# Kernel tuning notes

Hardware: AMD Instinct MI355X
Metric: run time of the kernel (lower is better)

Reference implementation:

```python
import jax, jax.numpy as jnp
import numpy as np

N = 100000   # nodes
E = 1600000  # edges
EPS = 1e-5


def _gcn_conv(x, W, b, src, dst, dinv):
    # PyG GCNConv with self-loops: out_i = sum_{j->i} d_j^-1/2 d_i^-1/2 (x_j W) + d_i^-1 (x_i W) + b
    h = x @ W                                   # [N, out]
    coef = dinv[src] * dinv[dst]                # [E]
    agg = jax.ops.segment_sum(h[src] * coef[:, None], dst, num_segments=N)
    agg = agg + h * (dinv * dinv)[:, None]      # self-loop term
    return agg + b


def _bn_eval(x, gamma, beta, mean, var):
    return (x - mean) * jax.lax.rsqrt(var + EPS) * gamma + beta


def setup_inputs() -> dict:
    key = jax.random.key(0)
    ks = jax.random.split(key, 8)
    F_IN, H, C = 128, 256, 32
    inp = {
        "x": jax.random.normal(ks[0], (N, F_IN), dtype=jnp.float32),
        "edge_index": jax.random.randint(ks[1], (2, E), 0, N, dtype=jnp.int64),
        # layer 1
        "W1": jax.random.normal(ks[2], (F_IN, H), dtype=jnp.float32) / np.sqrt(F_IN),
        "b1": jnp.zeros((H,), jnp.float32),
        "g1": jnp.ones((H,), jnp.float32),
        "be1": jnp.zeros((H,), jnp.float32),
        "m1": jax.random.normal(ks[3], (H,), dtype=jnp.float32) * 0.1,
        "v1": jnp.ones((H,), jnp.float32),
        # layer 2
        "W2": jax.random.normal(ks[4], (H, H), dtype=jnp.float32) / np.sqrt(H),
        "b2": jnp.zeros((H,), jnp.float32),
        "g2": jnp.ones((H,), jnp.float32),
        "be2": jnp.zeros((H,), jnp.float32),
        "m2": jax.random.normal(ks[5], (H,), dtype=jnp.float32) * 0.1,
        "v2": jnp.ones((H,), jnp.float32),
        # layer 3
        "W3": jax.random.normal(ks[6], (H, C), dtype=jnp.float32) / np.sqrt(H),
        "b3": jnp.zeros((C,), jnp.float32),
    }
    return inp


def reference(x, edge_index, W1, b1, g1, be1, m1, v1,
              W2, b2, g2, be2, m2, v2, W3, b3):
    src, dst = edge_index[0], edge_index[1]
    # degree with self-loops: in-degree + 1
    deg = jnp.zeros((N,), x.dtype).at[dst].add(1.0) + 1.0
    dinv = jax.lax.rsqrt(deg)

    h = _gcn_conv(x, W1, b1, src, dst, dinv)
    h = jax.nn.relu(_bn_eval(h, g1, be1, m1, v1))
    h = _gcn_conv(h, W2, b2, src, dst, dinv)
    h = jax.nn.relu(_bn_eval(h, g2, be2, m2, v2))
    h = _gcn_conv(h, W3, b3, src, dst, dinv)
    return jax.nn.sigmoid(h)
```

## Files before the change

kernel.cpp:

```cpp
#include <hip/hip_runtime.h>
#include <math.h>

typedef unsigned short u16;
typedef unsigned char u8;
typedef unsigned int u32;
typedef __attribute__((ext_vector_type(8))) __bf16 bfx8;
typedef __attribute__((ext_vector_type(4))) float f32x4;
typedef __attribute__((ext_vector_type(2))) float f32x2;
typedef __attribute__((ext_vector_type(8))) unsigned short us8;
typedef __attribute__((ext_vector_type(4))) unsigned short us4;

__device__ inline float bf2f(u16 u) {
    union { unsigned int i; float f; } v;
    v.i = ((unsigned int)u) << 16;
    return v.f;
}
__device__ inline u16 f2bf(float f) {
    union { float f; unsigned int i; } v;
    v.f = f;
    unsigned int b = v.i;
    return (u16)((b + 0x7FFFu + ((b >> 16) & 1u)) >> 16);
}
__device__ inline u32 bits_of(float f) {
    union { float f; u32 i; } v; v.f = f; return v.i;
}
__device__ inline u32 pkbf(float a, float b) {
    return (bits_of(a) >> 16) | (bits_of(b) & 0xffff0000u);
}
__device__ inline void dec4(u32 d, u32& lo, u32& hi) {
    f32x2 a = __builtin_amdgcn_cvt_pk_f32_fp8(d, false);
    f32x2 b = __builtin_amdgcn_cvt_pk_f32_fp8(d, true);
    lo = pkbf(a[0], a[1]);
    hi = pkbf(b[0], b[1]);
}


__global__ __launch_bounds__(256) void k_hist(const int* __restrict__ ei,
                                              u32* __restrict__ cnt_pb,
                                              int E, int NB, int NBLK) {
    __shared__ u32 h[256];
    int blk = blockIdx.x, tid = threadIdx.x;
    h[tid] = 0;
    __syncthreads();
    int eend = min(E, (blk + 1) * 2048);
    for (int e = blk * 2048 + tid; e < eend; e += 256) {
        int d = ei[E + e];
        atomicAdd(&h[d >> 9], 1u);
    }
    __syncthreads();
    if (tid < NB) cnt_pb[(size_t)tid * NBLK + blk] = h[tid];
}

__global__ __launch_bounds__(1024) void k_scanb(const u32* __restrict__ cnt_pb,
                                                u32* __restrict__ bases_pb,
                                                u32* __restrict__ bkt_tot,
                                                int NBLK) {
    __shared__ u32 lds[1024];
    int b = blockIdx.x, t = threadIdx.x;
    u32 v = (t < NBLK) ? cnt_pb[(size_t)b * NBLK + t] : 0u;
    lds[t] = v;
    __syncthreads();
    for (int off = 1; off < 1024; off <<= 1) {
        u32 x = lds[t];
        u32 y = (t >= off) ? lds[t - off] : 0u;
        __syncthreads();
        lds[t] = x + y;
        __syncthreads();
    }
    if (t < NBLK) bases_pb[(size_t)b * NBLK + t] = lds[t] - v;
    if (t == NBLK - 1) bkt_tot[b] = lds[t];
}

__global__ __launch_bounds__(256) void k_scatter2(const int* __restrict__ ei,
                                                  const u32* __restrict__ bases_pb,
                                                  const u32* __restrict__ bkt_tot,
                                                  u32* __restrict__ bkt_edges,
                                                  int E, int NB, int NBLK) {
    __shared__ u32 cur[256];
    __shared__ u32 bb[256];
    int blk = blockIdx.x, tid = threadIdx.x;
    u32 v = (tid < NB) ? bkt_tot[tid] : 0u;
    bb[tid] = v;
    __syncthreads();
    for (int off = 1; off < 256; off <<= 1) {
        u32 x = bb[tid];
        u32 y = (tid >= off) ? bb[tid - off] : 0u;
        __syncthreads();
        bb[tid] = x + y;
        __syncthreads();
    }
    u32 excl = bb[tid] - v;
    __syncthreads();
    bb[tid] = excl;
    if (tid < NB) cur[tid] = bases_pb[(size_t)tid * NBLK + blk];
    __syncthreads();
    int eend = min(E, (blk + 1) * 2048);
    for (int e = blk * 2048 + tid; e < eend; e += 256) {
        int s = ei[e];
        int d = ei[E + e];
        int b = d >> 9;
        int dl = d & 511;
        u32 off = atomicAdd(&cur[b], 1u);
        bkt_edges[bb[b] + off] = (u32)s | ((u32)dl << 17);
    }
}

__global__ __launch_bounds__(512) void k_bucket(const u32* __restrict__ bkt_edges,
                                                const u32* __restrict__ bkt_tot,
                                                int* __restrict__ row_ptr,
                                                float* __restrict__ dinv,
                                                int* __restrict__ csr_src,
                                                int N, int NB, int E) {
    __shared__ u32 sb[256];
    __shared__ u32 lcnt[512];
    __shared__ u32 lscan[512];
    int b = blockIdx.x, t = threadIdx.x;
    if (t < 256) sb[t] = (t < NB) ? bkt_tot[t] : 0u;
    __syncthreads();
    for (int off = 1; off < 256; off <<= 1) {
        u32 x = 0, y = 0;
        if (t < 256) { x = sb[t]; y = (t >= off) ? sb[t - off] : 0u; }
        __syncthreads();
        if (t < 256) sb[t] = x + y;
        __syncthreads();
    }
    int ce = (int)bkt_tot[b];
    int es = (int)sb[b] - ce;
    int node0 = b << 9;
    lcnt[t] = 0;
    __syncthreads();
    for (int i = t; i < ce; i += 512) {
        u32 p = bkt_edges[es + i];
        atomicAdd(&lcnt[p >> 17], 1u);
    }
    __syncthreads();
    lscan[t] = lcnt[t];
    __syncthreads();
    for (int off = 1; off < 512; off <<= 1) {
        u32 x = lscan[t];
        u32 y = (t >= off) ? lscan[t - off] : 0u;
        __syncthreads();
        lscan[t] = x + y;
        __syncthreads();
    }
    u32 excl = lscan[t] - lcnt[t];
    int node = node0 + t;
    if (node < N) {
        row_ptr[node] = es + (int)excl;
        dinv[node] = rsqrtf((float)lcnt[t] + 1.0f);
    }
    if (b == 0 && t == 0) row_ptr[N] = E;
    __syncthreads();
    lscan[t] = excl;
    __syncthreads();
    for (int i = t; i < ce; i += 512) {
        u32 p = bkt_edges[es + i];
        int dl = (int)(p >> 17);
        int src = (int)(p & 0x1FFFFu);
        u32 pos = atomicAdd(&lscan[dl], 1u);
        csr_src[es + pos] = src;
    }
}

__global__ __launch_bounds__(256) void k_prep(
    const float* __restrict__ x, u8* __restrict__ xq, const float* __restrict__ dinv, int n4,
    const float* __restrict__ W1, u16* __restrict__ Wt1,
    const float* __restrict__ W2, u16* __restrict__ Wt2,
    const float* __restrict__ W3, u16* __restrict__ Wt3,
    const float* __restrict__ b1, const float* __restrict__ g1, const float* __restrict__ be1,
    const float* __restrict__ m1, const float* __restrict__ v1,
    float* __restrict__ s1, float* __restrict__ t1,
    const float* __restrict__ b2, const float* __restrict__ g2, const float* __restrict__ be2,
    const float* __restrict__ m2, const float* __restrict__ v2,
    float* __restrict__ s2, float* __restrict__ t2)
{
    int i = blockIdx.x * blockDim.x + threadIdx.x;
    if (i < n4) {
        float d = dinv[i >> 5];
        float4 v = *(const float4*)(x + (size_t)i * 4);
        u32 pk = 0;
        pk = __builtin_amdgcn_cvt_pk_fp8_f32(v.x * d, v.y * d, pk, false);
        pk = __builtin_amdgcn_cvt_pk_fp8_f32(v.z * d, v.w * d, pk, true);
        *(u32*)(xq + (size_t)i * 4) = pk;
        return;
    }
    int j = i - n4;
    if (j < 128 * 256) {
        int k = j / 256, f = j % 256;
        Wt1[(size_t)f * 128 + k] = f2bf(W1[j]);
    } else if (j < 128 * 256 + 256 * 256) {
        int j2 = j - 128 * 256;
        int k = j2 / 256, f = j2 % 256;
        Wt2[(size_t)f * 256 + k] = f2bf(W2[j2]);
    } else if (j < 128 * 256 + 256 * 256 + 256 * 32) {
        int j3 = j - (128 * 256 + 256 * 256);
        int k = j3 / 32, f = j3 % 32;
        Wt3[(size_t)f * 256 + k] = f2bf(W3[j3]);
    } else {
        int k = j - (128 * 256 + 256 * 256 + 256 * 32);
        if (k < 256) {
            float sc = g1[k] * rsqrtf(v1[k] + 1e-5f);
            s1[k] = sc;
            t1[k] = (b1[k] - m1[k]) * sc + be1[k];
        } else if (k < 512) {
            int kk = k - 256;
            float sc = g2[kk] * rsqrtf(v2[kk] + 1e-5f);
            s2[kk] = sc;
            t2[kk] = (b2[kk] - m2[kk]) * sc + be2[kk];
        }
    }
}

template<int K, int FT, int MODE, bool AFP8, int MINW>
__global__ __launch_bounds__(256, MINW) void g_mfma_lds(
    const void* __restrict__ Av, const u16* __restrict__ Wt,
    void* __restrict__ Cv, int M, int Ftot,
    const float* __restrict__ s, const float* __restrict__ t,
    const float* __restrict__ dinv, int nTiles)
{
    constexpr bool DOBN = (MODE == 1) || (MODE == 3);
    constexpr bool CF8  = (MODE >= 3);
    constexpr int BK  = 128;
    constexpr int SA  = BK + 8;
    constexpr int NH  = K / BK;
    constexpr int NKH = BK / 32;
    constexpr int NF  = FT / 16;
    constexpr int EB  = CF8 ? 1 : 2;
    constexpr int SCB = FT * EB + 16;
    constexpr int EBa = AFP8 ? 1 : 2;
    constexpr int CR  = (BK * EBa) / 16;
    constexpr int LIT = (64 * CR) / 256;

    __shared__ u16 Asmem[2][64 * SA];
    __shared__ u8  Cs8[64 * SCB];

    const u8* Ab = (const u8*)Av;
    int tid = threadIdx.x;
    int w = tid >> 6, l = tid & 63;
    int lr = l & 15, koff8 = (l >> 4) * 8;
    int col0 = blockIdx.y * FT;

    bfx8 bfr[NH][NKH][NF];
    {
        const u16* wp = Wt + (size_t)(col0 + lr) * K + koff8;
        #pragma unroll
        for (int h = 0; h < NH; ++h)
            #pragma unroll
            for (int kk = 0; kk < NKH; ++kk)
                #pragma unroll
                for (int c = 0; c < NF; ++c)
                    bfr[h][kk][c] = *(const bfx8*)(wp + (size_t)c * 16 * K + h * BK + kk * 32);
    }

    int myT = (blockIdx.x < nTiles) ? ((nTiles - 1 - (int)blockIdx.x) / (int)gridDim.x + 1) : 0;
    int NM = myT * NH;
    if (NM == 0) return;

    f32x4 acc[NF];
    #pragma unroll
    for (int c = 0; c < NF; ++c) acc[c] = (f32x4){0.f, 0.f, 0.f, 0.f};

    uint4 rga[LIT];

    auto loadA = [&](int r0, int hh) {
        #pragma unroll
        for (int j = 0; j < LIT; ++j) {
            int cid = j * 256 + tid;
            int row = cid / CR, ch = cid % CR;
            int gr = r0 + row; if (gr > M - 1) gr = M - 1;
            rga[j] = *(const uint4*)(Ab + (size_t)gr * K * EBa + (size_t)hh * BK * EBa + ch * 16);
        }
    };
    auto writeA = [&](int buf) {
        #pragma unroll
        for (int j = 0; j < LIT; ++j) {
            int cid = j * 256 + tid;
            int row = cid / CR, ch = cid % CR;
            if (!AFP8) {
                *(uint4*)&Asmem[buf][row * SA + ch * 8] = rga[j];
            } else {
                u32 w0, w1, w2, w3, w4, w5, w6, w7;
                dec4(rga[j].x, w0, w1);
                dec4(rga[j].y, w2, w3);
                dec4(rga[j].z, w4, w5);
                dec4(rga[j].w, w6, w7);
                uint4 lo4; lo4.x = w0; lo4.y = w1; lo4.z = w2; lo4.w = w3;
                uint4 hi4; hi4.x = w4; hi4.y = w5; hi4.z = w6; hi4.w = w7;
                *(uint4*)&Asmem[buf][row * SA + ch * 16] = lo4;
                *(uint4*)&Asmem[buf][row * SA + ch * 16 + 8] = hi4;
            }
        }
    };

    loadA(blockIdx.x * 64, 0);
    writeA(0);
    if (NM > 1) {
        constexpr int gt1 = 1 / NH, h1 = 1 % NH;
        loadA((blockIdx.x + gt1 * gridDim.x) * 64, h1);
    }
    __syncthreads();

    int cur = 0, gm = 0;
    for (int ti = 0; ti < myT; ++ti) {
        int row0g = (blockIdx.x + ti * gridDim.x) * 64;
        #pragma unroll
        for (int h = 0; h < NH; ++h) {
            const u16* ab = &Asmem[cur][0];
            #pragma unroll
            for (int kk = 0; kk < NKH; ++kk) {
                bfx8 af = *(const bfx8*)(ab + (w * 16 + lr) * SA + koff8 + kk * 32);
                #pragma unroll
                for (int c = 0; c < NF; ++c)
                    acc[c] = __builtin_amdgcn_mfma_f32_16x16x32_bf16(af, bfr[h][kk][c], acc[c], 0, 0, 0);
            }
            if (h == NH - 1) {
                int orow = w * 16 + (l >> 4) * 4;
                float dr[4];
                #pragma unroll
                for (int r = 0; r < 4; ++r) {
                    int grow = row0g + orow + r;
                    dr[r] = DOBN ? ((grow < M) ? dinv[grow] : 0.f) : 1.f;
                }
                #pragma unroll
                for (int c = 0; c < NF; ++c) {
                    int gc = col0 + c * 16 + lr;
                    float sc = DOBN ? s[gc] : 0.f;
                    float tc = DOBN ? t[gc] : 0.f;
                    #pragma unroll
                    for (int r = 0; r < 4; ++r) {
                        float v = acc[c][r];
                        if (DOBN) v = fmaxf(v * sc + tc, 0.f) * dr[r];
                        if (CF8) {
                            int enc = __builtin_amdgcn_cvt_pk_fp8_f32(v, v, 0, false);
                            Cs8[(orow + r) * SCB + (c * 16 + lr)] = (u8)(enc & 0xff);
                        } else {
                            *(u16*)&Cs8[(orow + r) * SCB + (c * 16 + lr) * 2] = f2bf(v);
                        }
                    }
                    acc[c] = (f32x4){0.f, 0.f, 0.f, 0.f};
                }
            }
            __syncthreads();
            if (gm + 1 < NM) writeA(cur ^ 1);
            if (h == NH - 1) {
                constexpr int CPR = (FT * EB) / 16;
                constexpr int TOT = 64 * CPR;
                constexpr int CPT = (TOT + 255) / 256;
                u8* C8 = (u8*)Cv;
                #pragma unroll
                for (int j = 0; j < CPT; ++j) {
                    int cid = j * 256 + tid;
                    if (cid < TOT) {
                        int crow = cid / CPR;
                        int cb = (cid % CPR) * 16;
                        int grow = row0g + crow;
                        if (grow < M) {
                            us8 vv = *(const us8*)&Cs8[crow * SCB + cb];
                            *(us8*)(C8 + (size_t)grow * Ftot * EB + (size_t)col0 * EB + cb) = vv;
                        }
                    }
                }
            }
            if (gm + 2 < NM) {
                int g2 = gm + 2;
                int gt2 = g2 / NH, h2 = g2 % NH;
                loadA((blockIdx.x + gt2 * gridDim.x) * 64, h2);
            }
            __syncthreads();
            cur ^= 1; ++gm;
        }
    }
}

__global__ __launch_bounds__(256) void agg_x(const u8* __restrict__ in,
                                             u8* __restrict__ outp,
                                             const int* __restrict__ row_ptr,
                                             const int* __restrict__ csr_src,
                                             const float* __restrict__ dinv,
                                             int nnodes) {
    int tid = threadIdx.x;
    int wv = tid >> 6, lane = tid & 63;
    int half = lane >> 5, l32 = lane & 31;
    int node = (blockIdx.x * 4 + wv) * 2 + half;
    if (node >= nnodes) return;
    int off = l32 * 4;
    const u8* bp = in + off;
    float a0, a1, a2, a3;
    {
        u32 q = *(const u32*)(in + (size_t)node * 128 + off);
        f32x2 p;
        p = __builtin_amdgcn_cvt_pk_f32_fp8(q, false); a0 = p[0]; a1 = p[1];
        p = __builtin_amdgcn_cvt_pk_f32_fp8(q, true);  a2 = p[0]; a3 = p[1];
    }
    int e = row_ptr[node], e1 = row_ptr[node + 1];
    for (; e + 8 <= e1; e += 8) {
        int sx[8];
        #pragma unroll
        for (int q = 0; q < 8; ++q) sx[q] = csr_src[e + q];
        u32 vv[8];
        #pragma unroll
        for (int q = 0; q < 8; ++q) vv[q] = *(const u32*)(bp + (size_t)sx[q] * 128);
        #pragma unroll
        for (int q = 0; q < 8; ++q) {
            f32x2 p;
            p = __builtin_amdgcn_cvt_pk_f32_fp8(vv[q], false); a0 += p[0]; a1 += p[1];
            p = __builtin_amdgcn_cvt_pk_f32_fp8(vv[q], true);  a2 += p[0]; a3 += p[1];
        }
    }
    for (; e < e1; ++e) {
        int s0 = csr_src[e];
        u32 v0 = *(const u32*)(bp + (size_t)s0 * 128);
        f32x2 p;
        p = __builtin_amdgcn_cvt_pk_f32_fp8(v0, false); a0 += p[0]; a1 += p[1];
        p = __builtin_amdgcn_cvt_pk_f32_fp8(v0, true);  a2 += p[0]; a3 += p[1];
    }
    float d = dinv[node];
    u32 pk = 0;
    pk = __builtin_amdgcn_cvt_pk_fp8_f32(a0 * d, a1 * d, pk, false);
    pk = __builtin_amdgcn_cvt_pk_fp8_f32(a2 * d, a3 * d, pk, true);
    *(u32*)(outp + (size_t)node * 128 + off) = pk;
}

__global__ __launch_bounds__(256) void agg_h(const u8* __restrict__ in,
                                             u8* __restrict__ outp,
                                             const int* __restrict__ row_ptr,
                                             const int* __restrict__ csr_src,
                                             const float* __restrict__ dinv,
                                             int nnodes) {
    int tid = threadIdx.x;
    int wv = tid >> 6, lane = tid & 63;
    int half = lane >> 5, l32 = lane & 31;
    int node = (blockIdx.x * 4 + wv) * 2 + half;
    if (node >= nnodes) return;
    int off = l32 * 8;
    const u8* bp = in + off;
    float acc[8];
    {
        uint2 q = *(const uint2*)(in + (size_t)node * 256 + off);
        f32x2 p;
        p = __builtin_amdgcn_cvt_pk_f32_fp8(q.x, false); acc[0] = p[0]; acc[1] = p[1];
        p = __builtin_amdgcn_cvt_pk_f32_fp8(q.x, true);  acc[2] = p[0]; acc[3] = p[1];
        p = __builtin_amdgcn_cvt_pk_f32_fp8(q.y, false); acc[4] = p[0]; acc[5] = p[1];
        p = __builtin_amdgcn_cvt_pk_f32_fp8(q.y, true);  acc[6] = p[0]; acc[7] = p[1];
    }
    int e = row_ptr[node], e1 = row_ptr[node + 1];
    for (; e + 8 <= e1; e += 8) {
        int sx[8];
        #pragma unroll
        for (int q = 0; q < 8; ++q) sx[q] = csr_src[e + q];
        uint2 vv[8];
        #pragma unroll
        for (int q = 0; q < 8; ++q) vv[q] = *(const uint2*)(bp + (size_t)sx[q] * 256);
        #pragma unroll
        for (int q = 0; q < 8; ++q) {
            f32x2 p;
            p = __builtin_amdgcn_cvt_pk_f32_fp8(vv[q].x, false); acc[0] += p[0]; acc[1] += p[1];
            p = __builtin_amdgcn_cvt_pk_f32_fp8(vv[q].x, true);  acc[2] += p[0]; acc[3] += p[1];
            p = __builtin_amdgcn_cvt_pk_f32_fp8(vv[q].y, false); acc[4] += p[0]; acc[5] += p[1];
            p = __builtin_amdgcn_cvt_pk_f32_fp8(vv[q].y, true);  acc[6] += p[0]; acc[7] += p[1];
        }
    }
    for (; e < e1; ++e) {
        int s0 = csr_src[e];
        uint2 v0 = *(const uint2*)(bp + (size_t)s0 * 256);
        f32x2 p;
        p = __builtin_amdgcn_cvt_pk_f32_fp8(v0.x, false); acc[0] += p[0]; acc[1] += p[1];
        p = __builtin_amdgcn_cvt_pk_f32_fp8(v0.x, true);  acc[2] += p[0]; acc[3] += p[1];
        p = __builtin_amdgcn_cvt_pk_f32_fp8(v0.y, false); acc[4] += p[0]; acc[5] += p[1];
        p = __builtin_amdgcn_cvt_pk_f32_fp8(v0.y, true);  acc[6] += p[0]; acc[7] += p[1];
    }
    float d = dinv[node];
    u32 w0 = 0, w1 = 0;
    w0 = __builtin_amdgcn_cvt_pk_fp8_f32(acc[0] * d, acc[1] * d, w0, false);
    w0 = __builtin_amdgcn_cvt_pk_fp8_f32(acc[2] * d, acc[3] * d, w0, true);
    w1 = __builtin_amdgcn_cvt_pk_fp8_f32(acc[4] * d, acc[5] * d, w1, false);
    w1 = __builtin_amdgcn_cvt_pk_fp8_f32(acc[6] * d, acc[7] * d, w1, true);
    uint2 o; o.x = w0; o.y = w1;
    *(uint2*)(outp + (size_t)node * 256 + off) = o;
}

__global__ __launch_bounds__(256) void agg32_sig(const u8* __restrict__ zq,
                                                 float* __restrict__ out,
                                                 const int* __restrict__ row_ptr,
                                                 const int* __restrict__ csr_src,
                                                 const float* __restrict__ dinv,
                                                 const float* __restrict__ b3,
                                                 int nnodes) {
    int tid = threadIdx.x;
    int grp = tid >> 3, l8 = tid & 7;
    int node = blockIdx.x * 32 + grp;
    if (node >= nnodes) return;
    int off = l8 * 4;
    const u8* bp = zq + off;
    float a0, a1, a2, a3;
    {
        u32 q = *(const u32*)(zq + (size_t)node * 32 + off);
        f32x2 p;
        p = __builtin_amdgcn_cvt_pk_f32_fp8(q, false); a0 = p[0]; a1 = p[1];
        p = __builtin_amdgcn_cvt_pk_f32_fp8(q, true);  a2 = p[0]; a3 = p[1];
    }
    int e = row_ptr[node], e1 = row_ptr[node + 1];
    for (; e + 8 <= e1; e += 8) {
        int sx[8];
        #pragma unroll
        for (int q = 0; q < 8; ++q) sx[q] = csr_src[e + q];
        u32 vv[8];
        #pragma unroll
        for (int q = 0; q < 8; ++q) vv[q] = *(const u32*)(bp + (size_t)sx[q] * 32);
        #pragma unroll
        for (int q = 0; q < 8; ++q) {
            f32x2 p;
            p = __builtin_amdgcn_cvt_pk_f32_fp8(vv[q], false); a0 += p[0]; a1 += p[1];
            p = __builtin_amdgcn_cvt_pk_f32_fp8(vv[q], true);  a2 += p[0]; a3 += p[1];
        }
    }
    for (; e < e1; ++e) {
        int s0 = csr_src[e];
        u32 v0 = *(const u32*)(bp + (size_t)s0 * 32);
        f32x2 p;
        p = __builtin_amdgcn_cvt_pk_f32_fp8(v0, false); a0 += p[0]; a1 += p[1];
        p = __builtin_amdgcn_cvt_pk_f32_fp8(v0, true);  a2 += p[0]; a3 += p[1];
    }
    float d = dinv[node];
    int fb = l8 * 4;
    float4 o;
    o.x = 1.f / (1.f + expf(-(a0 * d + b3[fb + 0])));
    o.y = 1.f / (1.f + expf(-(a1 * d + b3[fb + 1])));
    o.z = 1.f / (1.f + expf(-(a2 * d + b3[fb + 2])));
    o.w = 1.f / (1.f + expf(-(a3 * d + b3[fb + 3])));
    *(float4*)(out + (size_t)node * 32 + fb) = o;
}


extern "C" void kernel_launch(void* const* d_in, const int* in_sizes, int n_in,
                              void* d_out, int out_size, void* d_ws, size_t ws_size,
                              hipStream_t stream) {
    const float* x  = (const float*)d_in[0];
    const int*   ei = (const int*)d_in[1];
    const float* W1 = (const float*)d_in[2];
    const float* b1 = (const float*)d_in[3];
    const float* g1 = (const float*)d_in[4];
    const float* be1 = (const float*)d_in[5];
    const float* m1 = (const float*)d_in[6];
    const float* v1 = (const float*)d_in[7];
    const float* W2 = (const float*)d_in[8];
    const float* b2 = (const float*)d_in[9];
    const float* g2 = (const float*)d_in[10];
    const float* be2 = (const float*)d_in[11];
    const float* m2 = (const float*)d_in[12];
    const float* v2 = (const float*)d_in[13];
    const float* W3 = (const float*)d_in[14];
    const float* b3 = (const float*)d_in[15];
    float* out = (float*)d_out;

    const int N = in_sizes[0] / 128;
    const int E = in_sizes[1] / 2;

    const int NB = (N + 511) >> 9;
    const int NBLK = (E + 2047) / 2048;

    char* w = (char*)d_ws;
    auto alloc = [&](size_t bytes) -> void* {
        void* p = (void*)w;
        w += (bytes + 255) & ~(size_t)255;
        return p;
    };
    int* row_ptr   = (int*)alloc((size_t)(N + 1) * 4);
    float* dinv    = (float*)alloc((size_t)N * 4);
    u32* cnt_pb    = (u32*)alloc((size_t)NB * NBLK * 4);
    u32* bases_pb  = (u32*)alloc((size_t)NB * NBLK * 4);
    u32* bkt_tot   = (u32*)alloc((size_t)NB * 4);
    u32* bkt_edges = (u32*)alloc((size_t)E * 4);
    float* s1 = (float*)alloc(256 * 4);
    float* t1 = (float*)alloc(256 * 4);
    float* s2 = (float*)alloc(256 * 4);
    float* t2 = (float*)alloc(256 * 4);
    u16* Wt1 = (u16*)alloc((size_t)128 * 256 * 2);
    u16* Wt2 = (u16*)alloc((size_t)256 * 256 * 2);
    u16* Wt3 = (u16*)alloc((size_t)256 * 32 * 2);
    int* csr_src = (int*)alloc((size_t)E * 4);
    u8*  xq   = (u8*)alloc((size_t)N * 128);
    u8*  xa   = (u8*)alloc((size_t)N * 128);
    u8*  h1q  = (u8*)alloc((size_t)N * 256);
    u8*  h1a  = (u8*)alloc((size_t)N * 256);
    u8*  h2q  = (u8*)alloc((size_t)N * 256);
    u8*  z3 = xq;

    int nT = (N + 63) / 64;
    int gagg = (N + 7) / 8;
    int n4 = N * 128 / 4;
    int prepTot = n4 + 128 * 256 + 256 * 256 + 256 * 32 + 512;

    k_hist<<<NBLK, 256, 0, stream>>>(ei, cnt_pb, E, NB, NBLK);
    k_scanb<<<NB, 1024, 0, stream>>>(cnt_pb, bases_pb, bkt_tot, NBLK);
    k_scatter2<<<NBLK, 256, 0, stream>>>(ei, bases_pb, bkt_tot, bkt_edges, E, NB, NBLK);
    k_bucket<<<NB, 512, 0, stream>>>(bkt_edges, bkt_tot, row_ptr, dinv, csr_src, N, NB, E);

    k_prep<<<(prepTot + 255) / 256, 256, 0, stream>>>(
        x, xq, dinv, n4, W1, Wt1, W2, Wt2, W3, Wt3,
        b1, g1, be1, m1, v1, s1, t1, b2, g2, be2, m2, v2, s2, t2);

    agg_x<<<gagg, 256, 0, stream>>>(xq, xa, row_ptr, csr_src, dinv, N);
    g_mfma_lds<128, 64, 3, true, 2><<<dim3(128, 4), 256, 0, stream>>>(
        (const void*)xa, Wt1, (void*)h1q, N, 256, s1, t1, dinv, nT);

    agg_h<<<gagg, 256, 0, stream>>>(h1q, h1a, row_ptr, csr_src, dinv, N);
    g_mfma_lds<256, 64, 3, true, 2><<<dim3(128, 4), 256, 0, stream>>>(
        (const void*)h1a, Wt2, (void*)h2q, N, 256, s2, t2, dinv, nT);

    g_mfma_lds<256, 32, 4, true, 2><<<dim3(512, 1), 256, 0, stream>>>(
        (const void*)h2q, Wt3, (void*)z3, N, 32, (const float*)nullptr,
        (const float*)nullptr, (const float*)nullptr, nT);
    agg32_sig<<<(N + 31) / 32, 256, 0, stream>>>(z3, out, row_ptr, csr_src, dinv, b3, N);
}
```

Baseline: 251.6 us.

## Fuse prep into hist/bucket kernels and pad aggregation tails with zero row

Moves weight transposition and BN folding into extra blocks of the histogram kernel, and moves the x fp8 quantization into the bucket kernel using the per-node dinv held in shared memory. This removes one kernel launch and a dependent pass over x. The aggregation kernels drop their scalar tail loops and instead pad each 8-edge batch with indices pointing at an extra zeroed row appended to each feature buffer. The padding adds wasted loads on partial batches, and the bucket kernel now does more serial work per block with only NB (~196) blocks converting x.

```diff
diff --git a/kernel.cpp b/kernel.cpp
--- a/kernel.cpp
+++ b/kernel.cpp
@@ -8,13 +8,7 @@
 typedef __attribute__((ext_vector_type(4))) float f32x4;
 typedef __attribute__((ext_vector_type(2))) float f32x2;
 typedef __attribute__((ext_vector_type(8))) unsigned short us8;
-typedef __attribute__((ext_vector_type(4))) unsigned short us4;
-
-__device__ inline float bf2f(u16 u) {
-    union { unsigned int i; float f; } v;
-    v.i = ((unsigned int)u) << 16;
-    return v.f;
-}
+
 __device__ inline u16 f2bf(float f) {
     union { float f; unsigned int i; } v;
     v.f = f;
@@ -35,11 +29,48 @@
 }
 
 
-__global__ __launch_bounds__(256) void k_hist(const int* __restrict__ ei,
-                                              u32* __restrict__ cnt_pb,
-                                              int E, int NB, int NBLK) {
+__global__ __launch_bounds__(256) void k_hist(
+    const int* __restrict__ ei, u32* __restrict__ cnt_pb, int E, int NB, int NBLK,
+    const float* __restrict__ W1, u16* __restrict__ Wt1,
+    const float* __restrict__ W2, u16* __restrict__ Wt2,
+    const float* __restrict__ W3, u16* __restrict__ Wt3,
+    const float* __restrict__ b1, const float* __restrict__ g1, const float* __restrict__ be1,
+    const float* __restrict__ m1, const float* __restrict__ v1,
+    float* __restrict__ s1, float* __restrict__ t1,
+    const float* __restrict__ b2, const float* __restrict__ g2, const float* __restrict__ be2,
+    const float* __restrict__ m2, const float* __restrict__ v2,
+    float* __restrict__ s2, float* __restrict__ t2)
+{
+    int blk = blockIdx.x, tid = threadIdx.x;
+    if (blk >= NBLK) {
+        int j = (blk - NBLK) * 256 + tid;
+        if (j < 128 * 256) {
+            int k = j / 256, f = j % 256;
+            Wt1[(size_t)f * 128 + k] = f2bf(W1[j]);
+        } else if (j < 128 * 256 + 256 * 256) {
+            int j2 = j - 128 * 256;
+            int k = j2 / 256, f = j2 % 256;
+            Wt2[(size_t)f * 256 + k] = f2bf(W2[j2]);
+        } else if (j < 128 * 256 + 256 * 256 + 256 * 32) {
+            int j3 = j - (128 * 256 + 256 * 256);
+            int k = j3 / 32, f = j3 % 32;
+            Wt3[(size_t)f * 256 + k] = f2bf(W3[j3]);
+        } else {
+            int k = j - (128 * 256 + 256 * 256 + 256 * 32);
+            if (k < 256) {
+                float sc = g1[k] * rsqrtf(v1[k] + 1e-5f);
+                s1[k] = sc;
+                t1[k] = (b1[k] - m1[k]) * sc + be1[k];
+            } else if (k < 512) {
+                int kk = k - 256;
+                float sc = g2[kk] * rsqrtf(v2[kk] + 1e-5f);
+                s2[kk] = sc;
+                t2[kk] = (b2[kk] - m2[kk]) * sc + be2[kk];
+            }
+        }
+        return;
+    }
     __shared__ u32 h[256];
-    int blk = blockIdx.x, tid = threadIdx.x;
     h[tid] = 0;
     __syncthreads();
     int eend = min(E, (blk + 1) * 2048);
@@ -110,6 +141,8 @@
                                                 int* __restrict__ row_ptr,
                                                 float* __restrict__ dinv,
                                                 int* __restrict__ csr_src,
+                                                const float* __restrict__ x,
+                                                u8* __restrict__ xq,
                                                 int N, int NB, int E) {
     __shared__ u32 sb[256];
     __shared__ u32 lcnt[512];
@@ -118,10 +151,10 @@
     if (t < 256) sb[t] = (t < NB) ? bkt_tot[t] : 0u;
     __syncthreads();
     for (int off = 1; off < 256; off <<= 1) {
-        u32 x = 0, y = 0;
-        if (t < 256) { x = sb[t]; y = (t >= off) ? sb[t - off] : 0u; }
-        __syncthreads();
-        if (t < 256) sb[t] = x + y;
+        u32 x0 = 0, y0 = 0;
+        if (t < 256) { x0 = sb[t]; y0 = (t >= off) ? sb[t - off] : 0u; }
+        __syncthreads();
+        if (t < 256) sb[t] = x0 + y0;
         __syncthreads();
     }
     int ce = (int)bkt_tot[b];
@@ -137,17 +170,18 @@
     lscan[t] = lcnt[t];
     __syncthreads();
     for (int off = 1; off < 512; off <<= 1) {
-        u32 x = lscan[t];
-        u32 y = (t >= off) ? lscan[t - off] : 0u;
-        __syncthreads();
-        lscan[t] = x + y;
+        u32 x0 = lscan[t];
+        u32 y0 = (t >= off) ? lscan[t - off] : 0u;
+        __syncthreads();
+        lscan[t] = x0 + y0;
         __syncthreads();
     }
     u32 excl = lscan[t] - lcnt[t];
     int node = node0 + t;
+    float my_d = rsqrtf((float)lcnt[t] + 1.0f);
     if (node < N) {
         row_ptr[node] = es + (int)excl;
-        dinv[node] = rsqrtf((float)lcnt[t] + 1.0f);
+        dinv[node] = my_d;
     }
     if (b == 0 && t == 0) row_ptr[N] = E;
     __syncthreads();
@@ -160,55 +194,23 @@
         u32 pos = atomicAdd(&lscan[dl], 1u);
         csr_src[es + pos] = src;
     }
-}
-
-__global__ __launch_bounds__(256) void k_prep(
-    const float* __restrict__ x, u8* __restrict__ xq, const float* __restrict__ dinv, int n4,
-    const float* __restrict__ W1, u16* __restrict__ Wt1,
-    const float* __restrict__ W2, u16* __restrict__ Wt2,
-    const float* __restrict__ W3, u16* __restrict__ Wt3,
-    const float* __restrict__ b1, const float* __restrict__ g1, const float* __restrict__ be1,
-    const float* __restrict__ m1, const float* __restrict__ v1,
-    float* __restrict__ s1, float* __restrict__ t1,
-    const float* __restrict__ b2, const float* __restrict__ g2, const float* __restrict__ be2,
-    const float* __restrict__ m2, const float* __restrict__ v2,
-    float* __restrict__ s2, float* __restrict__ t2)
-{
-    int i = blockIdx.x * blockDim.x + threadIdx.x;
-    if (i < n4) {
-        float d = dinv[i >> 5];
-        float4 v = *(const float4*)(x + (size_t)i * 4);
-        u32 pk = 0;
-        pk = __builtin_amdgcn_cvt_pk_fp8_f32(v.x * d, v.y * d, pk, false);
-        pk = __builtin_amdgcn_cvt_pk_fp8_f32(v.z * d, v.w * d, pk, true);
-        *(u32*)(xq + (size_t)i * 4) = pk;
-        return;
-    }
-    int j = i - n4;
-    if (j < 128 * 256) {
-        int k = j / 256, f = j % 256;
-        Wt1[(size_t)f * 128 + k] = f2bf(W1[j]);
-    } else if (j < 128 * 256 + 256 * 256) {
-        int j2 = j - 128 * 256;
-        int k = j2 / 256, f = j2 % 256;
-        Wt2[(size_t)f * 256 + k] = f2bf(W2[j2]);
-    } else if (j < 128 * 256 + 256 * 256 + 256 * 32) {
-        int j3 = j - (128 * 256 + 256 * 256);
-        int k = j3 / 32, f = j3 % 32;
-        Wt3[(size_t)f * 256 + k] = f2bf(W3[j3]);
-    } else {
-        int k = j - (128 * 256 + 256 * 256 + 256 * 32);
-        if (k < 256) {
-            float sc = g1[k] * rsqrtf(v1[k] + 1e-5f);
-            s1[k] = sc;
-            t1[k] = (b1[k] - m1[k]) * sc + be1[k];
-        } else if (k < 512) {
-            int kk = k - 256;
-            float sc = g2[kk] * rsqrtf(v2[kk] + 1e-5f);
-            s2[kk] = sc;
-            t2[kk] = (b2[kk] - m2[kk]) * sc + be2[kk];
-        }
-    }
+    __syncthreads();
+    ((float*)lcnt)[t] = my_d;
+    __syncthreads();
+    const float* df = (const float*)lcnt;
+    for (int i = t; i < 512 * 32; i += 512) {
+        int r = i >> 5;
+        int row = node0 + r;
+        if (row < N) {
+            float d = df[r];
+            float4 v = *(const float4*)(x + (size_t)row * 128 + (i & 31) * 4);
+            u32 pk = 0;
+            pk = __builtin_amdgcn_cvt_pk_fp8_f32(v.x * d, v.y * d, pk, false);
+            pk = __builtin_amdgcn_cvt_pk_fp8_f32(v.z * d, v.w * d, pk, true);
+            *(u32*)(xq + (size_t)row * 128 + (i & 31) * 4) = pk;
+        }
+    }
+    if (b == 0 && t < 32) *(u32*)(xq + (size_t)N * 128 + t * 4) = 0;
 }
 
 template<int K, int FT, int MODE, bool AFP8, int MINW>
@@ -239,6 +241,10 @@
     int w = tid >> 6, l = tid & 63;
     int lr = l & 15, koff8 = (l >> 4) * 8;
     int col0 = blockIdx.y * FT;
+
+    if (CF8 && blockIdx.x == 0 && blockIdx.y == 0) {
+        if (tid * 4 < Ftot) *(u32*)((u8*)Cv + (size_t)M * Ftot + tid * 4) = 0;
+    }
 
     bfx8 bfr[NH][NKH][NF];
     {
@@ -393,10 +399,14 @@
         p = __builtin_amdgcn_cvt_pk_f32_fp8(q, true);  a2 = p[0]; a3 = p[1];
     }
     int e = row_ptr[node], e1 = row_ptr[node + 1];
-    for (; e + 8 <= e1; e += 8) {
+    for (; e < e1; e += 8) {
         int sx[8];
         #pragma unroll
-        for (int q = 0; q < 8; ++q) sx[q] = csr_src[e + q];
+        for (int q = 0; q < 8; ++q) {
+            int ee = e + q;
+            int vsrc = csr_src[ee < e1 ? ee : e];
+            sx[q] = (ee < e1) ? vsrc : nnodes;
+        }
         u32 vv[8];
         #pragma unroll
         for (int q = 0; q < 8; ++q) vv[q] = *(const u32*)(bp + (size_t)sx[q] * 128);
@@ -406,13 +416,6 @@
             p = __builtin_amdgcn_cvt_pk_f32_fp8(vv[q], false); a0 += p[0]; a1 += p[1];
             p = __builtin_amdgcn_cvt_pk_f32_fp8(vv[q], true);  a2 += p[0]; a3 += p[1];
         }
-    }
-    for (; e < e1; ++e) {
-        int s0 = csr_src[e];
-        u32 v0 = *(const u32*)(bp + (size_t)s0 * 128);
-        f32x2 p;
-        p = __builtin_amdgcn_cvt_pk_f32_fp8(v0, false); a0 += p[0]; a1 += p[1];
-        p = __builtin_amdgcn_cvt_pk_f32_fp8(v0, true);  a2 += p[0]; a3 += p[1];
     }
     float d = dinv[node];
     u32 pk = 0;
@@ -444,10 +447,14 @@
         p = __builtin_amdgcn_cvt_pk_f32_fp8(q.y, true);  acc[6] = p[0]; acc[7] = p[1];
     }
     int e = row_ptr[node], e1 = row_ptr[node + 1];
-    for (; e + 8 <= e1; e += 8) {
+    for (; e < e1; e += 8) {
         int sx[8];
         #pragma unroll
-        for (int q = 0; q < 8; ++q) sx[q] = csr_src[e + q];
+        for (int q = 0; q < 8; ++q) {
+            int ee = e + q;
+            int vsrc = csr_src[ee < e1 ? ee : e];
+            sx[q] = (ee < e1) ? vsrc : nnodes;
+        }
         uint2 vv[8];
         #pragma unroll
         for (int q = 0; q < 8; ++q) vv[q] = *(const uint2*)(bp + (size_t)sx[q] * 256);
@@ -459,15 +466,6 @@
             p = __builtin_amdgcn_cvt_pk_f32_fp8(vv[q].y, false); acc[4] += p[0]; acc[5] += p[1];
             p = __builtin_amdgcn_cvt_pk_f32_fp8(vv[q].y, true);  acc[6] += p[0]; acc[7] += p[1];
         }
-    }
-    for (; e < e1; ++e) {
-        int s0 = csr_src[e];
-        uint2 v0 = *(const uint2*)(bp + (size_t)s0 * 256);
-        f32x2 p;
-        p = __builtin_amdgcn_cvt_pk_f32_fp8(v0.x, false); acc[0] += p[0]; acc[1] += p[1];
-        p = __builtin_amdgcn_cvt_pk_f32_fp8(v0.x, true);  acc[2] += p[0]; acc[3] += p[1];
-        p = __builtin_amdgcn_cvt_pk_f32_fp8(v0.y, false); acc[4] += p[0]; acc[5] += p[1];
-        p = __builtin_amdgcn_cvt_pk_f32_fp8(v0.y, true);  acc[6] += p[0]; acc[7] += p[1];
     }
     float d = dinv[node];
     u32 w0 = 0, w1 = 0;
@@ -500,10 +498,14 @@
         p = __builtin_amdgcn_cvt_pk_f32_fp8(q, true);  a2 = p[0]; a3 = p[1];
     }
     int e = row_ptr[node], e1 = row_ptr[node + 1];
-    for (; e + 8 <= e1; e += 8) {
+    for (; e < e1; e += 8) {
         int sx[8];
         #pragma unroll
-        for (int q = 0; q < 8; ++q) sx[q] = csr_src[e + q];
+        for (int q = 0; q < 8; ++q) {
+            int ee = e + q;
+            int vsrc = csr_src[ee < e1 ? ee : e];
+            sx[q] = (ee < e1) ? vsrc : nnodes;
+        }
         u32 vv[8];
         #pragma unroll
         for (int q = 0; q < 8; ++q) vv[q] = *(const u32*)(bp + (size_t)sx[q] * 32);
@@ -513,13 +515,6 @@
             p = __builtin_amdgcn_cvt_pk_f32_fp8(vv[q], false); a0 += p[0]; a1 += p[1];
             p = __builtin_amdgcn_cvt_pk_f32_fp8(vv[q], true);  a2 += p[0]; a3 += p[1];
         }
-    }
-    for (; e < e1; ++e) {
-        int s0 = csr_src[e];
-        u32 v0 = *(const u32*)(bp + (size_t)s0 * 32);
-        f32x2 p;
-        p = __builtin_amdgcn_cvt_pk_f32_fp8(v0, false); a0 += p[0]; a1 += p[1];
-        p = __builtin_amdgcn_cvt_pk_f32_fp8(v0, true);  a2 += p[0]; a3 += p[1];
     }
     float d = dinv[node];
     int fb = l8 * 4;
@@ -558,6 +553,7 @@
 
     const int NB = (N + 511) >> 9;
     const int NBLK = (E + 2047) / 2048;
+    const int PREPB = (128 * 256 + 256 * 256 + 256 * 32 + 512 + 255) / 256;
 
     char* w = (char*)d_ws;
     auto alloc = [&](size_t bytes) -> void* {
@@ -579,26 +575,23 @@
     u16* Wt2 = (u16*)alloc((size_t)256 * 256 * 2);
     u16* Wt3 = (u16*)alloc((size_t)256 * 32 * 2);
     int* csr_src = (int*)alloc((size_t)E * 4);
-    u8*  xq   = (u8*)alloc((size_t)N * 128);
+    u8*  xq   = (u8*)alloc((size_t)(N + 1) * 128);
     u8*  xa   = (u8*)alloc((size_t)N * 128);
-    u8*  h1q  = (u8*)alloc((size_t)N * 256);
+    u8*  h1q  = (u8*)alloc((size_t)(N + 1) * 256);
     u8*  h1a  = (u8*)alloc((size_t)N * 256);
-    u8*  h2q  = (u8*)alloc((size_t)N * 256);
+    u8*  h2q  = (u8*)alloc((size_t)(N + 1) * 256);
     u8*  z3 = xq;
 
     int nT = (N + 63) / 64;
     int gagg = (N + 7) / 8;
-    int n4 = N * 128 / 4;
-    int prepTot = n4 + 128 * 256 + 256 * 256 + 256 * 32 + 512;
-
-    k_hist<<<NBLK, 256, 0, stream>>>(ei, cnt_pb, E, NB, NBLK);
+
+    k_hist<<<NBLK + PREPB, 256, 0, stream>>>(ei, cnt_pb, E, NB, NBLK,
+        W1, Wt1, W2, Wt2, W3, Wt3,
+        b1, g1, be1, m1, v1, s1, t1, b2, g2, be2, m2, v2, s2, t2);
     k_scanb<<<NB, 1024, 0, stream>>>(cnt_pb, bases_pb, bkt_tot, NBLK);
     k_scatter2<<<NBLK, 256, 0, stream>>>(ei, bases_pb, bkt_tot, bkt_edges, E, NB, NBLK);
-    k_bucket<<<NB, 512, 0, stream>>>(bkt_edges, bkt_tot, row_ptr, dinv, csr_src, N, NB, E);
-
-    k_prep<<<(prepTot + 255) / 256, 256, 0, stream>>>(
-        x, xq, dinv, n4, W1, Wt1, W2, Wt2, W3, Wt3,
-        b1, g1, be1, m1, v1, s1, t1, b2, g2, be2, m2, v2, s2, t2);
+    k_bucket<<<NB, 512, 0, stream>>>(bkt_edges, bkt_tot, row_ptr, dinv, csr_src,
+                                     x, xq, N, NB, E);
 
     agg_x<<<gagg, 256, 0, stream>>>(xq, xa, row_ptr, csr_src, dinv, N);
     g_mfma_lds<128, 64, 3, true, 2><<<dim3(128, 4), 256, 0, stream>>>(
```

Result: faster. 231.3 us (-8.1%).
